# Optimization experiments

Hardware: AMD Instinct MI355X
Metric: run time of the kernel (lower is better)

Reference implementation:

```python
import jax, jax.numpy as jnp
import numpy as np

N_NODES = 30000
DEGREE = 16
HIDDEN = 128
MSG = 128


def setup_inputs() -> dict:
    key = jax.random.key(0)
    ks = jax.random.split(key, 16)
    coords = jax.random.normal(ks[0], (N_NODES, 3), dtype=jnp.float32)
    hidden = jax.random.normal(ks[1], (N_NODES, HIDDEN), dtype=jnp.float32)
    # fixed in-degree ring graph: unique (src,dst) pairs, in-degree == DEGREE for all nodes
    dst = jnp.repeat(jnp.arange(N_NODES, dtype=jnp.int64), DEGREE)
    off = jnp.tile(jnp.arange(1, DEGREE + 1, dtype=jnp.int64), N_NODES)
    src = (dst + off) % N_NODES
    edges = jnp.stack([src, dst], axis=0)  # [2, E]
    s = 0.05
    W1 = jax.random.normal(ks[2], (2 * HIDDEN + 1, MSG), dtype=jnp.float32) * s
    b1 = jnp.zeros((MSG,), jnp.float32)
    W2 = jax.random.normal(ks[3], (MSG, MSG), dtype=jnp.float32) * s
    b2 = jnp.zeros((MSG,), jnp.float32)
    Wa = jax.random.normal(ks[4], (MSG, 1), dtype=jnp.float32) * s
    ba = jnp.zeros((1,), jnp.float32)
    Wc1 = jax.random.normal(ks[5], (MSG, MSG), dtype=jnp.float32) * s
    bc1 = jnp.zeros((MSG,), jnp.float32)
    Wc2 = jax.random.normal(ks[6], (MSG, 1), dtype=jnp.float32) * s  # original zero-inits; random for nontrivial baseline
    Wh1 = jax.random.normal(ks[7], (HIDDEN + MSG, MSG), dtype=jnp.float32) * s
    bh1 = jnp.zeros((MSG,), jnp.float32)
    Wh2 = jax.random.normal(ks[8], (MSG, HIDDEN), dtype=jnp.float32) * s
    bh2 = jnp.zeros((HIDDEN,), jnp.float32)
    return dict(coords=coords, hidden=hidden, edges=edges, W1=W1, b1=b1, W2=W2, b2=b2,
                Wa=Wa, ba=ba, Wc1=Wc1, bc1=bc1, Wc2=Wc2, Wh1=Wh1, bh1=bh1, Wh2=Wh2, bh2=bh2)


def reference(coords, hidden, edges, W1, b1, W2, b2, Wa, ba, Wc1, bc1, Wc2, Wh1, bh1, Wh2, bh2):
    n = coords.shape[0]
    src, dst = edges[0], edges[1]
    coords_dif = coords[src] - coords[dst]                      # [E,3]
    l2 = jnp.linalg.norm(coords_dif, axis=1, keepdims=True)     # [E,1]
    x = jnp.concatenate([hidden[src], hidden[dst], l2], axis=1)  # [E, 2h+1]
    m = jnp.tanh(x @ W1 + b1)
    m = jnp.tanh(m @ W2 + b2)                                   # m_ij [E,MSG]
    m = jax.nn.sigmoid(m @ Wa + ba) * m                          # attention gate
    c = jnp.tanh(m @ Wc1 + bc1)
    c = jnp.tanh(c @ Wc2)                                       # [E,1] (Tanh since has_attention)
    coord_trans = coords_dif * c                                 # [E,3]
    # dense [N,N,*] scatter + sum over dim 0 == segment-sum over edges[1] (unique edges)
    trans_sum = jax.ops.segment_sum(coord_trans, dst, num_segments=n)  # [N,3]
    indeg = jax.ops.segment_sum(jnp.ones_like(dst, dtype=coords.dtype), dst, num_segments=n)
    coords_out = coords + trans_sum / indeg[:, None]
    m_i = jax.ops.segment_sum(m, dst, num_segments=n)            # [N,MSG]
    h = jnp.tanh(jnp.concatenate([hidden, m_i], axis=1) @ Wh1 + bh1)
    h = h @ Wh2 + bh2
    hidden_out = hidden + h
    return coords_out, hidden_out
```

## Files before the change

### kernel.cpp

```cpp
#include <hip/hip_runtime.h>
#include <hip/hip_bf16.h>
#include <math.h>


typedef __attribute__((ext_vector_type(8))) short short8;
typedef __attribute__((ext_vector_type(4))) float f32x4;
typedef __attribute__((ext_vector_type(4))) unsigned int u32x4;

#define MFMA __builtin_amdgcn_mfma_f32_16x16x32_bf16

#define OFF_W1A_HI 0
#define OFF_W1A_LO 16384
#define OFF_W1B_HI 32768
#define OFF_W1B_LO 49152
#define OFF_W2_HI  65536
#define OFF_WC1_HI 81920
#define OFF_WH1_HI 98304
#define OFF_WH1_LO 131072
#define OFF_WH2_HI 163840
#define FRAG_TOTAL 180224

__device__ __align__(16) unsigned short g_frags[FRAG_TOTAL];

#define DEVFN static __device__ __forceinline__

DEVFN unsigned short f2bf(float x) {
  unsigned int u = __float_as_uint(x);
  u += 0x7fffu + ((u >> 16) & 1u);
  return (unsigned short)(u >> 16);
}
DEVFN float bf2f(unsigned short h) { return __uint_as_float(((unsigned int)h) << 16); }

DEVFN unsigned int pk2(float a, float b) {
  __hip_bfloat162 p = __float22bfloat162_rn(make_float2(a, b));
  union { __hip_bfloat162 h; unsigned int u; } cv;
  cv.h = p;
  return cv.u;
}

DEVFN float fexp2(float x) {
  float r;
  asm volatile("v_exp_f32 %0, %1" : "=v"(r) : "v"(x));
  return r;
}
DEVFN float frcp(float x) {
  float r;
  asm volatile("v_rcp_f32 %0, %1" : "=v"(r) : "v"(x));
  return r;
}
DEVFN float ftanh(float x) {
  return 1.0f - 2.0f * frcp(fexp2(x * 2.8853900817779268f) + 1.0f);
}
DEVFN float fsigmoid(float x) {
  return frcp(1.0f + fexp2(-x * 1.4426950408889634f));
}

DEVFN void mk8(const float* __restrict__ x, short8& hi, short8& lo) {
  unsigned int hp[4], lp[4];
#pragma unroll
  for (int q = 0; q < 4; ++q) hp[q] = pk2(x[2 * q], x[2 * q + 1]);
#pragma unroll
  for (int q = 0; q < 4; ++q) {
    float f0 = __uint_as_float(hp[q] << 16);
    float f1 = __uint_as_float(hp[q] & 0xffff0000u);
    lp[q] = pk2(x[2 * q] - f0, x[2 * q + 1] - f1);
  }
  union { u32x4 u; short8 s; } ch, clo;
  ch.u[0] = hp[0]; ch.u[1] = hp[1]; ch.u[2] = hp[2]; ch.u[3] = hp[3];
  clo.u[0] = lp[0]; clo.u[1] = lp[1]; clo.u[2] = lp[2]; clo.u[3] = lp[3];
  hi = ch.s; lo = clo.s;
}

DEVFN short8 bfrag(int off_u16, int kt, int nt, int lane) {
  return *(const short8*)(g_frags + off_u16 + (((kt << 3) + nt) << 9) + (lane << 3));
}

DEVFN short8 xs_read(const unsigned short* Xs, int row, int sbyte) {
  return *(const short8*)((const char*)Xs + row * 256 + (sbyte ^ ((row & 7) << 4)));
}
DEVFN void xs_write8(unsigned short* Xs, int row, int cl, const float* v) {
  u32x4 w;
  w[0] = pk2(v[0], v[1]); w[1] = pk2(v[2], v[3]);
  w[2] = pk2(v[4], v[5]); w[3] = pk2(v[6], v[7]);
  *(u32x4*)((char*)Xs + row * 256 + ((cl << 4) ^ ((row & 7) << 4))) = w;
}
DEVFN void xs_write4(unsigned short* Xs, int row, int byte0, const float* v) {
  uint2 w;
  w.x = pk2(v[0], v[1]); w.y = pk2(v[2], v[3]);
  *(uint2*)((char*)Xs + row * 256 + (byte0 ^ ((row & 7) << 4))) = w;
}

#define ZERO8 { _Pragma("unroll") for (int nt = 0; nt < 8; ++nt) acc[nt] = vzero; }
#define ZERO4(a) { _Pragma("unroll") for (int q = 0; q < 4; ++q) (a)[q] = vzero; }

__global__ __launch_bounds__(256) void wconv_kernel(const float* __restrict__ W1,
                                                    const float* __restrict__ W2,
                                                    const float* __restrict__ Wc1,
                                                    const float* __restrict__ Wh1,
                                                    const float* __restrict__ Wh2) {
  int t = blockIdx.x * 256 + threadIdx.x;
  if (t >= 28 * 4096) return;
  int seg = t >> 12, r = t & 4095;
  int j = r & 7, lane = (r >> 3) & 63, nt = (r >> 9) & 7;
  int kg = lane >> 4, cl = lane & 15;
  const float* src; int kt, offH, offL, perm;
  if (seg < 4)       { src = W1;             kt = seg;      offH = OFF_W1A_HI; offL = OFF_W1A_LO; perm = 0; }
  else if (seg < 8)  { src = W1 + 128 * 128; kt = seg - 4;  offH = OFF_W1B_HI; offL = OFF_W1B_LO; perm = 0; }
  else if (seg < 12) { src = W2;             kt = seg - 8;  offH = OFF_W2_HI;  offL = -1;         perm = 1; }
  else if (seg < 16) { src = Wc1;            kt = seg - 12; offH = OFF_WC1_HI; offL = -1;         perm = 1; }
  else if (seg < 24) { src = Wh1;            kt = seg - 16; offH = OFF_WH1_HI; offL = OFF_WH1_LO; perm = 0; }
  else               { src = Wh2;            kt = seg - 24; offH = OFF_WH2_HI; offL = -1;         perm = 1; }
  int ke = kt * 32 + kg * 8 + j;
  int k = perm ? ((ke & 7) * 16 + (ke >> 3)) : ke;
  float w = src[k * 128 + nt * 16 + cl];
  unsigned short h = f2bf(w);
  int fi = kt * 4096 + nt * 512 + lane * 8 + j;
  g_frags[offH + fi] = h;
  if (offL >= 0) g_frags[offL + fi] = f2bf(w - bf2f(h));
}

__global__ __launch_bounds__(256) void st_kernel(const float* __restrict__ hidden,
                                                 const float* __restrict__ b1,
                                                 float* __restrict__ S,
                                                 float* __restrict__ T, int N) {
  const int tid = threadIdx.x, wid = tid >> 6, lane = tid & 63;
  const int cl = lane & 15, kg = lane >> 4;
  const int rg = wid >> 1, nh = wid & 1;
  const int n0 = blockIdx.x * 32 + rg * 16;
  const float* Arow = hidden + ((size_t)min(n0 + cl, N - 1) << 7);
  const f32x4 vzero = {0.f, 0.f, 0.f, 0.f};
  f32x4 accS[4], accT[4];
  ZERO4(accS); ZERO4(accT);
#pragma unroll
  for (int ks = 0; ks < 4; ++ks) {
    float x[8];
    *(f32x4*)&x[0] = *(const f32x4*)(Arow + ks * 32 + kg * 8);
    *(f32x4*)&x[4] = *(const f32x4*)(Arow + ks * 32 + kg * 8 + 4);
    short8 ah, al;
    mk8(x, ah, al);
#pragma unroll
    for (int q = 0; q < 4; ++q) {
      int nt = nh * 4 + q;
      short8 bh = bfrag(OFF_W1A_HI, ks, nt, lane);
      short8 bl = bfrag(OFF_W1A_LO, ks, nt, lane);
      accS[q] = MFMA(ah, bh, accS[q], 0, 0, 0);
      accS[q] = MFMA(al, bh, accS[q], 0, 0, 0);
      accS[q] = MFMA(ah, bl, accS[q], 0, 0, 0);
      bh = bfrag(OFF_W1B_HI, ks, nt, lane);
      bl = bfrag(OFF_W1B_LO, ks, nt, lane);
      accT[q] = MFMA(ah, bh, accT[q], 0, 0, 0);
      accT[q] = MFMA(al, bh, accT[q], 0, 0, 0);
      accT[q] = MFMA(ah, bl, accT[q], 0, 0, 0);
    }
  }
#pragma unroll
  for (int q = 0; q < 4; ++q) {
    int nt = nh * 4 + q;
    float bv = b1[nt * 16 + cl];
#pragma unroll
    for (int reg = 0; reg < 4; ++reg) {
      int rw = n0 + kg * 4 + reg;
      if (rw < N) {
        size_t o = (size_t)rw * 128 + nt * 16 + cl;
        S[o] = accS[q][reg];
        T[o] = accT[q][reg] + bv;
      }
    }
  }
}

__global__ __launch_bounds__(256) void edge_kernel(
    const float* __restrict__ coords, const int* __restrict__ edges,
    const float* __restrict__ W1, const float* __restrict__ b2,
    const float* __restrict__ Wa, const float* __restrict__ ba,
    const float* __restrict__ bc1, const float* __restrict__ Wc2,
    const float* __restrict__ T, const float* __restrict__ S,
    unsigned short* __restrict__ Mh, unsigned short* __restrict__ Ml,
    float* __restrict__ coords_out, int E) {
  __shared__ __align__(16) unsigned short Xs[64 * 128];
  __shared__ float swl2f[128], swaf[128], swc2f[128], sb2f[128], sbc1f[128];

  const int tid = threadIdx.x, wid = tid >> 6, lane = tid & 63;
  const int cl = lane & 15, kg = lane >> 4;
  const int xrow0 = wid * 16;
  const int e0 = blockIdx.x * 64 + wid * 16;

  if (tid < 128) {
    swl2f[tid] = W1[256 * 128 + tid];
    swaf[tid] = Wa[tid];
    swc2f[tid] = Wc2[tid];
    sb2f[tid] = b2[tid];
    sbc1f[tid] = bc1[tid];
  }
  __syncthreads();

  const int dst = edges[E + e0];
  const int src = edges[e0 + cl];
  const float cx = coords[3 * dst], cy = coords[3 * dst + 1], cz = coords[3 * dst + 2];
  const float dx = coords[3 * src] - cx, dy = coords[3 * src + 1] - cy, dz = coords[3 * src + 2] - cz;
  const float l2 = sqrtf(dx * dx + dy * dy + dz * dz);
  const float ba_s = ba[0];

  const f32x4 vzero = {0.f, 0.f, 0.f, 0.f};
  f32x4 acc[8];

  {
    const float* Trow = T + (size_t)dst * 128;
    const float* Srow[4];
    float l2r[4];
#pragma unroll
    for (int reg = 0; reg < 4; ++reg) {
      Srow[reg] = S + ((size_t)__shfl(src, kg * 4 + reg) << 7);
      l2r[reg] = __shfl(l2, kg * 4 + reg);
    }
    float vv[4][8];
#pragma unroll
    for (int nt = 0; nt < 8; ++nt) {
      const int c = nt * 16 + cl;
      float tv = Trow[c];
      float wl = swl2f[c];
#pragma unroll
      for (int reg = 0; reg < 4; ++reg)
        vv[reg][nt] = ftanh(Srow[reg][c] + tv + l2r[reg] * wl);
    }
#pragma unroll
    for (int reg = 0; reg < 4; ++reg) xs_write8(Xs, xrow0 + kg * 4 + reg, cl, vv[reg]);
  }

  ZERO8;
#pragma unroll
  for (int ks = 0; ks < 4; ++ks) {
    short8 a = xs_read(Xs, xrow0 + cl, ks * 64 + kg * 16);
#pragma unroll
    for (int nt = 0; nt < 8; ++nt) {
      short8 b = bfrag(OFF_W2_HI, ks, nt, lane);
      acc[nt] = MFMA(a, b, acc[nt], 0, 0, 0);
    }
  }

  {
    float wac[8], b2c[8];
#pragma unroll
    for (int nt = 0; nt < 8; ++nt) {
      wac[nt] = swaf[nt * 16 + cl];
      b2c[nt] = sb2f[nt * 16 + cl];
    }
#pragma unroll
    for (int nt = 0; nt < 8; ++nt)
#pragma unroll
      for (int reg = 0; reg < 4; ++reg)
        acc[nt][reg] = ftanh(acc[nt][reg] + b2c[nt]);
    float p[4];
#pragma unroll
    for (int reg = 0; reg < 4; ++reg) {
      float s = 0.f;
#pragma unroll
      for (int nt = 0; nt < 8; ++nt) s = fmaf(acc[nt][reg], wac[nt], s);
      p[reg] = s;
    }
#pragma unroll
    for (int m = 1; m <= 8; m <<= 1)
#pragma unroll
      for (int reg = 0; reg < 4; ++reg) p[reg] += __shfl_xor(p[reg], m);
    float g[4];
#pragma unroll
    for (int reg = 0; reg < 4; ++reg) g[reg] = fsigmoid(p[reg] + ba_s);
#pragma unroll
    for (int nt = 0; nt < 8; ++nt)
#pragma unroll
      for (int reg = 0; reg < 4; ++reg) acc[nt][reg] *= g[reg];
    float cs[8];
#pragma unroll
    for (int nt = 0; nt < 8; ++nt) {
      cs[nt] = (acc[nt][0] + acc[nt][1]) + (acc[nt][2] + acc[nt][3]);
      cs[nt] += __shfl_xor(cs[nt], 16);
      cs[nt] += __shfl_xor(cs[nt], 32);
    }
    if (lane < 16) {
      size_t base = (size_t)dst * 128 + lane;
#pragma unroll
      for (int nt = 0; nt < 8; ++nt) {
        float s = cs[nt];
        unsigned short hh = f2bf(s);
        Mh[base + nt * 16] = hh;
        Ml[base + nt * 16] = f2bf(s - bf2f(hh));
      }
    }
    float vv[4][8];
#pragma unroll
    for (int nt = 0; nt < 8; ++nt)
#pragma unroll
      for (int reg = 0; reg < 4; ++reg) vv[reg][nt] = acc[nt][reg];
#pragma unroll
    for (int reg = 0; reg < 4; ++reg) xs_write8(Xs, xrow0 + kg * 4 + reg, cl, vv[reg]);
  }

  ZERO8;
#pragma unroll
  for (int ks = 0; ks < 4; ++ks) {
    short8 a = xs_read(Xs, xrow0 + cl, ks * 64 + kg * 16);
#pragma unroll
    for (int nt = 0; nt < 8; ++nt) {
      short8 b = bfrag(OFF_WC1_HI, ks, nt, lane);
      acc[nt] = MFMA(a, b, acc[nt], 0, 0, 0);
    }
  }

  {
    float wcc[8], bcc[8];
#pragma unroll
    for (int nt = 0; nt < 8; ++nt) {
      wcc[nt] = swc2f[nt * 16 + cl];
      bcc[nt] = sbc1f[nt * 16 + cl];
    }
    float p[4];
#pragma unroll
    for (int reg = 0; reg < 4; ++reg) {
      float s = 0.f;
#pragma unroll
      for (int nt = 0; nt < 8; ++nt)
        s = fmaf(ftanh(acc[nt][reg] + bcc[nt]), wcc[nt], s);
      p[reg] = s;
    }
#pragma unroll
    for (int m = 1; m <= 8; m <<= 1)
#pragma unroll
      for (int reg = 0; reg < 4; ++reg) p[reg] += __shfl_xor(p[reg], m);
    float st = 0.f;
#pragma unroll
    for (int reg = 0; reg < 4; ++reg) {
      int sl = kg * 4 + reg;
      float vx = __shfl(dx, sl), vy = __shfl(dy, sl), vz = __shfl(dz, sl);
      float cmp = ((cl & 3) == 1) ? vy : (((cl & 3) == 2) ? vz : vx);
      st = fmaf(cmp, ftanh(p[reg]), st);
    }
    st += __shfl_xor(st, 16);
    st += __shfl_xor(st, 32);
    if (lane < 3)
      coords_out[dst * 3 + lane] = coords[dst * 3 + lane] + st * 0.0625f;
  }
}

__global__ __launch_bounds__(256) void node_kernel(
    const float* __restrict__ hidden, const unsigned short* __restrict__ Mh,
    const unsigned short* __restrict__ Ml, const float* __restrict__ bh1,
    const float* __restrict__ bh2, float* __restrict__ hidden_out, int N) {
  __shared__ __align__(16) unsigned short Xs[32 * 128];
  const int tid = threadIdx.x, wid = tid >> 6, lane = tid & 63;
  const int cl = lane & 15, kg = lane >> 4;
  const int rg = wid >> 1, nh = wid & 1;
  const int n0 = blockIdx.x * 32 + rg * 16;
  const int rmin = min(n0 + cl, N - 1);
  const f32x4 vzero = {0.f, 0.f, 0.f, 0.f};
  f32x4 acc[4];
  ZERO4(acc);
  {
    const float* Arow = hidden + ((size_t)rmin << 7);
#pragma unroll
    for (int ks = 0; ks < 4; ++ks) {
      float x[8];
      *(f32x4*)&x[0] = *(const f32x4*)(Arow + ks * 32 + kg * 8);
      *(f32x4*)&x[4] = *(const f32x4*)(Arow + ks * 32 + kg * 8 + 4);
      short8 ah, al;
      mk8(x, ah, al);
#pragma unroll
      for (int q = 0; q < 4; ++q) {
        int nt = nh * 4 + q;
        short8 bh = bfrag(OFF_WH1_HI, ks, nt, lane);
        short8 bl = bfrag(OFF_WH1_LO, ks, nt, lane);
        acc[q] = MFMA(ah, bh, acc[q], 0, 0, 0);
        acc[q] = MFMA(al, bh, acc[q], 0, 0, 0);
        acc[q] = MFMA(ah, bl, acc[q], 0, 0, 0);
      }
    }
  }
  {
    const int prow = rmin << 7;
#pragma unroll
    for (int ks = 0; ks < 4; ++ks) {
      short8 ah = *(const short8*)(Mh + prow + ks * 32 + kg * 8);
      short8 al = *(const short8*)(Ml + prow + ks * 32 + kg * 8);
#pragma unroll
      for (int q = 0; q < 4; ++q) {
        int nt = nh * 4 + q;
        short8 bh = bfrag(OFF_WH1_HI, 4 + ks, nt, lane);
        short8 bl = bfrag(OFF_WH1_LO, 4 + ks, nt, lane);
        acc[q] = MFMA(ah, bh, acc[q], 0, 0, 0);
        acc[q] = MFMA(al, bh, acc[q], 0, 0, 0);
        acc[q] = MFMA(ah, bl, acc[q], 0, 0, 0);
      }
    }
  }
  {
    float vv[4][4];
#pragma unroll
    for (int q = 0; q < 4; ++q) {
      float bv = bh1[(nh * 4 + q) * 16 + cl];
#pragma unroll
      for (int reg = 0; reg < 4; ++reg) vv[reg][q] = ftanh(acc[q][reg] + bv);
    }
#pragma unroll
    for (int reg = 0; reg < 4; ++reg)
      xs_write4(Xs, rg * 16 + kg * 4 + reg, cl * 16 + nh * 8, vv[reg]);
  }
  __syncthreads();
  ZERO4(acc);
#pragma unroll
  for (int ks = 0; ks < 4; ++ks) {
    short8 a = xs_read(Xs, rg * 16 + cl, ks * 64 + kg * 16);
#pragma unroll
    for (int q = 0; q < 4; ++q) {
      short8 b = bfrag(OFF_WH2_HI, ks, nh * 4 + q, lane);
      acc[q] = MFMA(a, b, acc[q], 0, 0, 0);
    }
  }
#pragma unroll
  for (int q = 0; q < 4; ++q) {
    int nt = nh * 4 + q;
    float bv = bh2[nt * 16 + cl];
#pragma unroll
    for (int reg = 0; reg < 4; ++reg) {
      int rw = n0 + kg * 4 + reg;
      if (rw < N) {
        size_t o = (size_t)rw * 128 + nt * 16 + cl;
        hidden_out[o] = hidden[o] + acc[q][reg] + bv;
      }
    }
  }
}

extern "C" void kernel_launch(void* const* d_in, const int* in_sizes, int n_in,
                              void* d_out, int out_size, void* d_ws, size_t ws_size,
                              hipStream_t stream) {
  const float* coords = (const float*)d_in[0];
  const float* hidden = (const float*)d_in[1];
  const int* edges = (const int*)d_in[2];
  const float* W1 = (const float*)d_in[3];
  const float* b1 = (const float*)d_in[4];
  const float* W2 = (const float*)d_in[5];
  const float* b2 = (const float*)d_in[6];
  const float* Wa = (const float*)d_in[7];
  const float* ba = (const float*)d_in[8];
  const float* Wc1 = (const float*)d_in[9];
  const float* bc1 = (const float*)d_in[10];
  const float* Wc2 = (const float*)d_in[11];
  const float* Wh1 = (const float*)d_in[12];
  const float* bh1 = (const float*)d_in[13];
  const float* Wh2 = (const float*)d_in[14];
  const float* bh2 = (const float*)d_in[15];

  const int N = in_sizes[0] / 3;
  const int E = in_sizes[2] / 2;

  float* T = (float*)d_ws;
  float* S = T + (size_t)N * 128;
  unsigned short* Mh = (unsigned short*)(S + (size_t)N * 128);
  unsigned short* Ml = Mh + (size_t)N * 128;
  float* coords_out = (float*)d_out;
  float* hidden_out = coords_out + (size_t)N * 3;

  wconv_kernel<<<448, 256, 0, stream>>>(W1, W2, Wc1, Wh1, Wh2);
  const int nb32 = (N + 31) / 32;
  st_kernel<<<nb32, 256, 0, stream>>>(hidden, b1, S, T, N);
  edge_kernel<<<E / 64, 256, 0, stream>>>(coords, edges, W1, b2, Wa, ba, bc1, Wc2,
                                          T, S, Mh, Ml, coords_out, E);
  node_kernel<<<nb32, 256, 0, stream>>>(hidden, Mh, Ml, bh1, bh2, hidden_out, N);
}
```

Measured before the change: 286.9 us.

## Vectorize edge S/T gather, re-tile node/st kernels to 16 rows, spread M stores

The edge kernel's first layer now has each lane load contiguous 32-float chunks of its own edge's S and T rows as float4 vectors, replacing the scalar strided column gathers. This requires a different column order, so W2's fragment permutation is switched off. The st and node kernels move to 16-row blocks with each wave owning two output tiles, which doubles the grid and halves LDS use. M_i stores are spread across all four lane groups instead of only the first 16 lanes.

```diff
diff --git a/kernel.cpp b/kernel.cpp
--- a/kernel.cpp
+++ b/kernel.cpp
@@ -84,14 +84,9 @@
   w[2] = pk2(v[4], v[5]); w[3] = pk2(v[6], v[7]);
   *(u32x4*)((char*)Xs + row * 256 + ((cl << 4) ^ ((row & 7) << 4))) = w;
 }
-DEVFN void xs_write4(unsigned short* Xs, int row, int byte0, const float* v) {
-  uint2 w;
-  w.x = pk2(v[0], v[1]); w.y = pk2(v[2], v[3]);
-  *(uint2*)((char*)Xs + row * 256 + (byte0 ^ ((row & 7) << 4))) = w;
-}
 
 #define ZERO8 { _Pragma("unroll") for (int nt = 0; nt < 8; ++nt) acc[nt] = vzero; }
-#define ZERO4(a) { _Pragma("unroll") for (int q = 0; q < 4; ++q) (a)[q] = vzero; }
+#define ZERO2(a) { _Pragma("unroll") for (int q = 0; q < 2; ++q) (a)[q] = vzero; }
 
 __global__ __launch_bounds__(256) void wconv_kernel(const float* __restrict__ W1,
                                                     const float* __restrict__ W2,
@@ -106,7 +101,7 @@
   const float* src; int kt, offH, offL, perm;
   if (seg < 4)       { src = W1;             kt = seg;      offH = OFF_W1A_HI; offL = OFF_W1A_LO; perm = 0; }
   else if (seg < 8)  { src = W1 + 128 * 128; kt = seg - 4;  offH = OFF_W1B_HI; offL = OFF_W1B_LO; perm = 0; }
-  else if (seg < 12) { src = W2;             kt = seg - 8;  offH = OFF_W2_HI;  offL = -1;         perm = 1; }
+  else if (seg < 12) { src = W2;             kt = seg - 8;  offH = OFF_W2_HI;  offL = -1;         perm = 0; }
   else if (seg < 16) { src = Wc1;            kt = seg - 12; offH = OFF_WC1_HI; offL = -1;         perm = 1; }
   else if (seg < 24) { src = Wh1;            kt = seg - 16; offH = OFF_WH1_HI; offL = OFF_WH1_LO; perm = 0; }
   else               { src = Wh2;            kt = seg - 24; offH = OFF_WH2_HI; offL = -1;         perm = 1; }
@@ -125,12 +120,11 @@
                                                  float* __restrict__ T, int N) {
   const int tid = threadIdx.x, wid = tid >> 6, lane = tid & 63;
   const int cl = lane & 15, kg = lane >> 4;
-  const int rg = wid >> 1, nh = wid & 1;
-  const int n0 = blockIdx.x * 32 + rg * 16;
+  const int n0 = blockIdx.x * 16;
   const float* Arow = hidden + ((size_t)min(n0 + cl, N - 1) << 7);
   const f32x4 vzero = {0.f, 0.f, 0.f, 0.f};
-  f32x4 accS[4], accT[4];
-  ZERO4(accS); ZERO4(accT);
+  f32x4 accS[2], accT[2];
+  ZERO2(accS); ZERO2(accT);
 #pragma unroll
   for (int ks = 0; ks < 4; ++ks) {
     float x[8];
@@ -139,8 +133,8 @@
     short8 ah, al;
     mk8(x, ah, al);
 #pragma unroll
-    for (int q = 0; q < 4; ++q) {
-      int nt = nh * 4 + q;
+    for (int q = 0; q < 2; ++q) {
+      int nt = wid * 2 + q;
       short8 bh = bfrag(OFF_W1A_HI, ks, nt, lane);
       short8 bl = bfrag(OFF_W1A_LO, ks, nt, lane);
       accS[q] = MFMA(ah, bh, accS[q], 0, 0, 0);
@@ -154,8 +148,8 @@
     }
   }
 #pragma unroll
-  for (int q = 0; q < 4; ++q) {
-    int nt = nh * 4 + q;
+  for (int q = 0; q < 2; ++q) {
+    int nt = wid * 2 + q;
     float bv = b1[nt * 16 + cl];
 #pragma unroll
     for (int reg = 0; reg < 4; ++reg) {
@@ -178,7 +172,8 @@
     unsigned short* __restrict__ Mh, unsigned short* __restrict__ Ml,
     float* __restrict__ coords_out, int E) {
   __shared__ __align__(16) unsigned short Xs[64 * 128];
-  __shared__ float swl2f[128], swaf[128], swc2f[128], sb2f[128], sbc1f[128];
+  __shared__ __align__(16) float swl2f[128];
+  __shared__ float swaf[128], swc2f[128], sb2f[128], sbc1f[128];
 
   const int tid = threadIdx.x, wid = tid >> 6, lane = tid & 63;
   const int cl = lane & 15, kg = lane >> 4;
@@ -205,26 +200,35 @@
   f32x4 acc[8];
 
   {
-    const float* Trow = T + (size_t)dst * 128;
-    const float* Srow[4];
-    float l2r[4];
-#pragma unroll
-    for (int reg = 0; reg < 4; ++reg) {
-      Srow[reg] = S + ((size_t)__shfl(src, kg * 4 + reg) << 7);
-      l2r[reg] = __shfl(l2, kg * 4 + reg);
-    }
-    float vv[4][8];
-#pragma unroll
-    for (int nt = 0; nt < 8; ++nt) {
-      const int c = nt * 16 + cl;
-      float tv = Trow[c];
-      float wl = swl2f[c];
-#pragma unroll
-      for (int reg = 0; reg < 4; ++reg)
-        vv[reg][nt] = ftanh(Srow[reg][c] + tv + l2r[reg] * wl);
-    }
-#pragma unroll
-    for (int reg = 0; reg < 4; ++reg) xs_write8(Xs, xrow0 + kg * 4 + reg, cl, vv[reg]);
+    const int cb = kg;
+    const float* Sr = S + ((size_t)src << 7) + cb * 32;
+    const float* Tr = T + ((size_t)dst << 7) + cb * 32;
+    const float* Wr = swl2f + cb * 32;
+#pragma unroll
+    for (int q = 0; q < 4; ++q) {
+      f32x4 s0 = *(const f32x4*)(Sr + q * 8);
+      f32x4 s1 = *(const f32x4*)(Sr + q * 8 + 4);
+      f32x4 t0 = *(const f32x4*)(Tr + q * 8);
+      f32x4 t1 = *(const f32x4*)(Tr + q * 8 + 4);
+      f32x4 w0 = *(const f32x4*)(Wr + q * 8);
+      f32x4 w1 = *(const f32x4*)(Wr + q * 8 + 4);
+      u32x4 w;
+      float v0, v1;
+      v0 = ftanh(s0[0] + t0[0] + l2 * w0[0]);
+      v1 = ftanh(s0[1] + t0[1] + l2 * w0[1]);
+      w[0] = pk2(v0, v1);
+      v0 = ftanh(s0[2] + t0[2] + l2 * w0[2]);
+      v1 = ftanh(s0[3] + t0[3] + l2 * w0[3]);
+      w[1] = pk2(v0, v1);
+      v0 = ftanh(s1[0] + t1[0] + l2 * w1[0]);
+      v1 = ftanh(s1[1] + t1[1] + l2 * w1[1]);
+      w[2] = pk2(v0, v1);
+      v0 = ftanh(s1[2] + t1[2] + l2 * w1[2]);
+      v1 = ftanh(s1[3] + t1[3] + l2 * w1[3]);
+      w[3] = pk2(v0, v1);
+      int row = xrow0 + cl;
+      *(u32x4*)((char*)Xs + row * 256 + ((cb * 64 + q * 16) ^ ((row & 7) << 4))) = w;
+    }
   }
 
   ZERO8;
@@ -276,10 +280,12 @@
       cs[nt] += __shfl_xor(cs[nt], 16);
       cs[nt] += __shfl_xor(cs[nt], 32);
     }
-    if (lane < 16) {
-      size_t base = (size_t)dst * 128 + lane;
-#pragma unroll
-      for (int nt = 0; nt < 8; ++nt) {
+    {
+      int g4 = lane >> 4;
+      size_t base = (size_t)dst * 128 + cl;
+#pragma unroll
+      for (int e2 = 0; e2 < 2; ++e2) {
+        int nt = g4 * 2 + e2;
         float s = cs[nt];
         unsigned short hh = f2bf(s);
         Mh[base + nt * 16] = hh;
@@ -345,15 +351,14 @@
     const float* __restrict__ hidden, const unsigned short* __restrict__ Mh,
     const unsigned short* __restrict__ Ml, const float* __restrict__ bh1,
     const float* __restrict__ bh2, float* __restrict__ hidden_out, int N) {
-  __shared__ __align__(16) unsigned short Xs[32 * 128];
+  __shared__ __align__(16) unsigned short Xs[16 * 128];
   const int tid = threadIdx.x, wid = tid >> 6, lane = tid & 63;
   const int cl = lane & 15, kg = lane >> 4;
-  const int rg = wid >> 1, nh = wid & 1;
-  const int n0 = blockIdx.x * 32 + rg * 16;
+  const int n0 = blockIdx.x * 16;
   const int rmin = min(n0 + cl, N - 1);
   const f32x4 vzero = {0.f, 0.f, 0.f, 0.f};
-  f32x4 acc[4];
-  ZERO4(acc);
+  f32x4 acc[2];
+  ZERO2(acc);
   {
     const float* Arow = hidden + ((size_t)rmin << 7);
 #pragma unroll
@@ -364,8 +369,8 @@
       short8 ah, al;
       mk8(x, ah, al);
 #pragma unroll
-      for (int q = 0; q < 4; ++q) {
-        int nt = nh * 4 + q;
+      for (int q = 0; q < 2; ++q) {
+        int nt = wid * 2 + q;
         short8 bh = bfrag(OFF_WH1_HI, ks, nt, lane);
         short8 bl = bfrag(OFF_WH1_LO, ks, nt, lane);
         acc[q] = MFMA(ah, bh, acc[q], 0, 0, 0);
@@ -381,8 +386,8 @@
       short8 ah = *(const short8*)(Mh + prow + ks * 32 + kg * 8);
       short8 al = *(const short8*)(Ml + prow + ks * 32 + kg * 8);
 #pragma unroll
-      for (int q = 0; q < 4; ++q) {
-        int nt = nh * 4 + q;
+      for (int q = 0; q < 2; ++q) {
+        int nt = wid * 2 + q;
         short8 bh = bfrag(OFF_WH1_HI, 4 + ks, nt, lane);
         short8 bl = bfrag(OFF_WH1_LO, 4 + ks, nt, lane);
         acc[q] = MFMA(ah, bh, acc[q], 0, 0, 0);
@@ -392,31 +397,29 @@
     }
   }
   {
-    float vv[4][4];
-#pragma unroll
-    for (int q = 0; q < 4; ++q) {
-      float bv = bh1[(nh * 4 + q) * 16 + cl];
-#pragma unroll
-      for (int reg = 0; reg < 4; ++reg) vv[reg][q] = ftanh(acc[q][reg] + bv);
-    }
-#pragma unroll
-    for (int reg = 0; reg < 4; ++reg)
-      xs_write4(Xs, rg * 16 + kg * 4 + reg, cl * 16 + nh * 8, vv[reg]);
+    float bv0 = bh1[(wid * 2 + 0) * 16 + cl];
+    float bv1 = bh1[(wid * 2 + 1) * 16 + cl];
+#pragma unroll
+    for (int reg = 0; reg < 4; ++reg) {
+      int row = kg * 4 + reg;
+      unsigned int w = pk2(ftanh(acc[0][reg] + bv0), ftanh(acc[1][reg] + bv1));
+      *(unsigned int*)((char*)Xs + row * 256 + ((cl * 16 + wid * 4) ^ ((row & 7) << 4))) = w;
+    }
   }
   __syncthreads();
-  ZERO4(acc);
+  ZERO2(acc);
 #pragma unroll
   for (int ks = 0; ks < 4; ++ks) {
-    short8 a = xs_read(Xs, rg * 16 + cl, ks * 64 + kg * 16);
-#pragma unroll
-    for (int q = 0; q < 4; ++q) {
-      short8 b = bfrag(OFF_WH2_HI, ks, nh * 4 + q, lane);
+    short8 a = xs_read(Xs, cl, ks * 64 + kg * 16);
+#pragma unroll
+    for (int q = 0; q < 2; ++q) {
+      short8 b = bfrag(OFF_WH2_HI, ks, wid * 2 + q, lane);
       acc[q] = MFMA(a, b, acc[q], 0, 0, 0);
     }
   }
 #pragma unroll
-  for (int q = 0; q < 4; ++q) {
-    int nt = nh * 4 + q;
+  for (int q = 0; q < 2; ++q) {
+    int nt = wid * 2 + q;
     float bv = bh2[nt * 16 + cl];
 #pragma unroll
     for (int reg = 0; reg < 4; ++reg) {
@@ -460,9 +463,9 @@
   float* hidden_out = coords_out + (size_t)N * 3;
 
   wconv_kernel<<<448, 256, 0, stream>>>(W1, W2, Wc1, Wh1, Wh2);
-  const int nb32 = (N + 31) / 32;
-  st_kernel<<<nb32, 256, 0, stream>>>(hidden, b1, S, T, N);
+  const int nb16 = (N + 15) / 16;
+  st_kernel<<<nb16, 256, 0, stream>>>(hidden, b1, S, T, N);
   edge_kernel<<<E / 64, 256, 0, stream>>>(coords, edges, W1, b2, Wa, ba, bc1, Wc2,
                                           T, S, Mh, Ml, coords_out, E);
-  node_kernel<<<nb32, 256, 0, stream>>>(hidden, Mh, Ml, bh1, bh2, hidden_out, N);
-}
+  node_kernel<<<nb16, 256, 0, stream>>>(hidden, Mh, Ml, bh1, bh2, hidden_out, N);
+}
```

Result: faster. 256.3 us (-10.7%).
